# Performance work log

Hardware: AMD Instinct MI355X
Metric: run time of the kernel (lower is better)

## Reference

```python
import jax, jax.numpy as jnp
import numpy as np

MAX_LENGTH = 25
SOS_TOKEN = 0


def setup_inputs() -> dict:
    key = jax.random.key(0)
    B, S, H, V = 32, 50, 256, 50257
    ks = jax.random.split(key, 16)
    u = lambda k, shape, fan: jax.random.uniform(k, shape, jnp.float32, -1.0, 1.0) / np.sqrt(fan)
    return {
        "encoder_hidden": jax.random.normal(ks[0], (1, B, H), jnp.float32),
        "encoder_outputs": jax.random.normal(ks[1], (B, S, H), jnp.float32),
        "target_tensor": jax.random.randint(ks[2], (B, MAX_LENGTH), 0, V),
        "embedding": jax.random.normal(ks[3], (V, H), jnp.float32) * 0.02,
        "Wa_w": u(ks[4], (H, H), H), "Wa_b": u(ks[5], (H,), H),
        "Ua_w": u(ks[6], (H, H), H), "Ua_b": u(ks[7], (H,), H),
        "Va_w": u(ks[8], (1, H), H), "Va_b": u(ks[9], (1,), H),
        "gru_w_ih": u(ks[10], (3 * H, 2 * H), H), "gru_b_ih": u(ks[11], (3 * H,), H),
        "gru_w_hh": u(ks[12], (3 * H, H), H), "gru_b_hh": u(ks[13], (3 * H,), H),
        "out_w": u(ks[14], (V, H), H), "out_b": u(ks[15], (V,), H),
    }


def reference(encoder_hidden, encoder_outputs, target_tensor, embedding,
              Wa_w, Wa_b, Ua_w, Ua_b, Va_w, Va_b,
              gru_w_ih, gru_b_ih, gru_w_hh, gru_b_hh, out_w, out_b):
    B, S, H = encoder_outputs.shape
    keys = encoder_outputs
    # Ua(keys) is step-invariant: precompute.  [B,S,H]
    ua_keys = jnp.einsum("bsh,gh->bsg", keys, Ua_w) + Ua_b
    # teacher-forced input tokens: [SOS, target[:, :-1]] -> [T,B]
    toks = jnp.concatenate(
        [jnp.full((B, 1), SOS_TOKEN, dtype=target_tensor.dtype),
         target_tensor[:, : MAX_LENGTH - 1]], axis=1).T

    def step(h, tok):
        # h: [B,H], tok: [B]
        emb = embedding[tok]                                   # [B,H]
        # Bahdanau attention (dropout is identity in eval mode)
        wa_q = h @ Wa_w.T + Wa_b                               # [B,H]
        e = jnp.tanh(wa_q[:, None, :] + ua_keys)               # [B,S,H]
        scores = jnp.einsum("bsh,h->bs", e, Va_w[0]) + Va_b[0]  # [B,S]
        w = jax.nn.softmax(scores, axis=-1)                    # [B,S]
        ctx = jnp.einsum("bs,bsh->bh", w, keys)                # [B,H]
        # GRU cell (PyTorch gate order: r, z, n)
        x = jnp.concatenate([emb, ctx], axis=-1)               # [B,2H]
        gi = x @ gru_w_ih.T + gru_b_ih                         # [B,3H]
        gh = h @ gru_w_hh.T + gru_b_hh                         # [B,3H]
        ir, iz, inn = jnp.split(gi, 3, axis=-1)
        hr, hz, hn = jnp.split(gh, 3, axis=-1)
        r = jax.nn.sigmoid(ir + hr)
        z = jax.nn.sigmoid(iz + hz)
        n = jnp.tanh(inn + r * hn)
        h2 = (1.0 - z) * n + z * h
        logits = h2 @ out_w.T + out_b                          # [B,V]
        return h2, (logits, w)

    h0 = encoder_hidden[0]                                     # [B,H]
    hT, (logits, attn) = jax.lax.scan(step, h0, toks)          # [T,B,V], [T,B,S]
    dec_out = jax.nn.log_softmax(logits.transpose(1, 0, 2), axis=-1)  # [B,T,V]
    attentions = attn.transpose(1, 0, 2)                       # [B,T,S]
    return dec_out, hT[None], attentions
```

## Files before the change

### kernel.cpp

```cpp
#include <hip/hip_runtime.h>
#include <math.h>

#define B_ 32
#define S_ 50
#define H_ 256
#define T_ 25
#define V_ 50257
#define VP 50260
#define NCH 786
#define NROW (B_ * T_)
#define NWROW 1024
#define VT_ 3144
#define MROW 54
#define SOS 0

typedef unsigned short ushort_t;
typedef __attribute__((ext_vector_type(8))) unsigned short ushort8;
typedef __attribute__((ext_vector_type(8))) short short8v;
typedef __attribute__((ext_vector_type(4))) float f32x4;

__device__ ushort_t g_ua[B_ * S_ * H_];
__device__ ushort_t g_hbf[NROW * H_];
__device__ float    g_gie[T_ * B_ * 3 * H_];
__device__ ushort_t g_wpk[(size_t)VT_ * 32 * 16 * 8];
__device__ ushort_t g_wcat[NWROW * H_];
__device__ ushort_t g_MT2[B_ * 768 * MROW];
__device__ ushort_t g_lgt[(size_t)NROW * VP];
__device__ float    g_pmax[NROW * NCH];
__device__ float    g_psum[NROW * NCH];

__device__ __forceinline__ float bf2f(ushort_t h) {
  union { unsigned int u; float f; } c; c.u = ((unsigned int)h) << 16; return c.f;
}
__device__ __forceinline__ ushort_t f2bf(float f) {
  union { float f; unsigned int u; } c; c.f = f;
  unsigned int u = c.u;
  return (ushort_t)((u + 0x7FFFu + ((u >> 16) & 1u)) >> 16);
}
__device__ __forceinline__ float tanh_fast(float x) {
  const float e = __expf(2.f * x);
  return 1.f - 2.f / (e + 1.f);
}

__global__ void k_pre(const float* __restrict__ keys, const float* __restrict__ Ua_w,
                      const float* __restrict__ Ua_b, const float* __restrict__ Wa_b,
                      const float* __restrict__ W_hh, const float* __restrict__ Wa_w,
                      const float* __restrict__ W_ih, const float* __restrict__ b_ih,
                      const int* __restrict__ tgt, const float* __restrict__ emb_tab) {
  __shared__ float sbuf[S_ * H_];
  const int bid = blockIdx.x, tid = threadIdx.x;

  if (bid < B_ * S_) {
    sbuf[tid] = keys[bid * H_ + tid];
    __syncthreads();
    float acc = Ua_b[tid] + Wa_b[tid];
    const float4* wrow = (const float4*)(Ua_w + (size_t)tid * H_);
    const float4* sk4 = (const float4*)sbuf;
    for (int k = 0; k < H_ / 4; ++k) {
      const float4 w = wrow[k], x = sk4[k];
      acc += w.x * x.x + w.y * x.y + w.z * x.z + w.w * x.w;
    }
    g_ua[(size_t)bid * H_ + tid] = f2bf(acc);
  } else if (bid < 1984) {
    const int cc = bid - 1600;
    const int c = cc % 12, b = cc / 12;
    {
      const float4* src = (const float4*)(keys + (size_t)b * S_ * H_);
      float4* dst = (float4*)sbuf;
      for (int i = tid; i < S_ * H_ / 4; i += 256) dst[i] = src[i];
    }
    __syncthreads();
    const int sub = tid & 15, grp = tid >> 4;
#pragma unroll 1
    for (int it = 0; it < 4; ++it) {
      const int j = c * 64 + it * 16 + grp;
      float w16[16];
#pragma unroll
      for (int kp = 0; kp < 16; ++kp)
        w16[kp] = W_ih[(size_t)j * (2 * H_) + H_ + sub + 16 * kp];
#pragma unroll 1
      for (int s = 0; s < S_; ++s) {
        float a = 0.f;
#pragma unroll
        for (int kp = 0; kp < 16; ++kp) a += w16[kp] * sbuf[s * H_ + sub + 16 * kp];
        a += __shfl_xor(a, 8); a += __shfl_xor(a, 4);
        a += __shfl_xor(a, 2); a += __shfl_xor(a, 1);
        if (sub == 0) g_MT2[(size_t)b * 768 * MROW + j * MROW + s] = f2bf(a);
      }
    }
  } else if (bid < 2284) {
    const int cc = bid - 1984;
    const int chunk = cc % 12, t = cc / 12;
    for (int i = tid; i < B_ * H_; i += 256) {
      const int b = i >> 8, g = i & 255;
      const int tok = (t == 0) ? SOS : tgt[b * T_ + (t - 1)];
      sbuf[i] = emb_tab[(size_t)tok * H_ + g];
    }
    __syncthreads();
    const int vl = tid & 63, wd = tid >> 6;
    const int j = chunk * 64 + vl;
    const float4* wrow = (const float4*)(W_ih + (size_t)j * (2 * H_));
    const float4* se4 = (const float4*)sbuf;
    float acc[8];
    const float base = b_ih[j];
#pragma unroll
    for (int bb = 0; bb < 8; ++bb) acc[bb] = base;
    for (int k4 = 0; k4 < 64; ++k4) {
      const float4 w = wrow[k4];
#pragma unroll
      for (int bb = 0; bb < 8; ++bb) {
        const float4 x = se4[(wd * 8 + bb) * 64 + k4];
        acc[bb] += w.x * x.x + w.y * x.y + w.z * x.z + w.w * x.w;
      }
    }
#pragma unroll
    for (int bb = 0; bb < 8; ++bb)
      g_gie[((size_t)t * B_ + (wd * 8 + bb)) * (3 * H_) + j] = acc[bb];
  } else {
    const size_t i0 = (size_t)(bid - 2284) * 256 + tid;
    for (size_t i = i0; i < (size_t)NWROW * H_; i += 256u * 256u) {
      const int r = (int)(i >> 8), k = (int)(i & 255);
      const float v = (r < 256) ? Wa_w[r * H_ + k] : W_hh[(r - 256) * H_ + k];
      g_wcat[i] = f2bf(v);
    }
  }
}

__global__ void __launch_bounds__(1024, 1)
k_recur(const float* __restrict__ enc_h, const float* __restrict__ Va_w,
        const float* __restrict__ Va_b, const float* __restrict__ b_hh,
        const float* __restrict__ out_w, float* __restrict__ out) {
  __shared__ ushort_t s_ua[S_ * H_];
  __shared__ ushort_t s_M[768 * MROW];
  __shared__ float s_res[NWROW];
  __shared__ float s_mw[768];
  __shared__ float s_h[H_];
  __shared__ float s_va[H_];
  __shared__ float s_score[64], s_w[64];
  const int bidx = blockIdx.x, tid = threadIdx.x;

  if (bidx >= 32) {
    const size_t total = (size_t)VT_ * 32 * 16;
    for (size_t p = (size_t)(bidx - 32) * 1024 + tid; p < total;
         p += (size_t)(gridDim.x - 32) * 1024) {
      const int c = (int)(p & 15);
      const int kg = (int)((p >> 4) & 31);
      const int vt = (int)(p >> 9);
      const int v = vt * 16 + c;
      short8v val = {0, 0, 0, 0, 0, 0, 0, 0};
      if (v < V_) {
        const float4* owr = (const float4*)(out_w + (size_t)v * H_ + kg * 8);
        const float4 f0 = owr[0], f1 = owr[1];
        val[0] = (short)f2bf(f0.x); val[1] = (short)f2bf(f0.y);
        val[2] = (short)f2bf(f0.z); val[3] = (short)f2bf(f0.w);
        val[4] = (short)f2bf(f1.x); val[5] = (short)f2bf(f1.y);
        val[6] = (short)f2bf(f1.z); val[7] = (short)f2bf(f1.w);
      }
      ((short8v*)g_wpk)[p] = val;
    }
    return;
  }

  const int b = bidx;
  const int lane = tid & 63, wid = tid >> 6;
  const int sub = lane & 15;
  const int grp = tid >> 4;

  {
    const uint4* src = (const uint4*)(g_ua + (size_t)b * S_ * H_);
    uint4* dst = (uint4*)s_ua;
    for (int i = tid; i < S_ * H_ / 8; i += 1024) dst[i] = src[i];
    const uint4* src2 = (const uint4*)(g_MT2 + (size_t)b * 768 * MROW);
    uint4* dst2 = (uint4*)s_M;
    for (int i = tid; i < 768 * MROW / 8; i += 1024) dst2[i] = src2[i];
  }
  float hreg = 0.f, bhh0 = 0.f, bhh1 = 0.f, bhh2 = 0.f;
  if (tid < H_) {
    hreg = enc_h[b * H_ + tid];
    s_h[tid] = hreg;
    s_va[tid] = Va_w[tid];
    bhh0 = b_hh[tid]; bhh1 = b_hh[H_ + tid]; bhh2 = b_hh[2 * H_ + tid];
  }
  if (tid >= 50 && tid < 64) s_w[tid] = 0.f;
  const float vab = Va_b[0];
  __syncthreads();

  for (int t = 0; t < T_; ++t) {
    float gie0 = 0.f, gie1 = 0.f, gie2 = 0.f;
    if (tid < H_) {
      const float* gp = g_gie + ((size_t)t * B_ + b) * (3 * H_);
      gie0 = gp[tid]; gie1 = gp[H_ + tid]; gie2 = gp[2 * H_ + tid];
    }

#pragma unroll 4
    for (int it = 0; it < 16; ++it) {
      const int row = it * 64 + grp;
      const ushort8* wr = (const ushort8*)(g_wcat + (size_t)row * H_);
      const ushort8 w0 = wr[sub], w1 = wr[16 + sub];
      const float* v0 = s_h + sub * 8;
      const float* v1 = s_h + 128 + sub * 8;
      float a0 = 0.f, a1 = 0.f;
#pragma unroll
      for (int j = 0; j < 8; ++j) { a0 += bf2f(w0[j]) * v0[j]; a1 += bf2f(w1[j]) * v1[j]; }
      float a = a0 + a1;
      a += __shfl_xor(a, 8); a += __shfl_xor(a, 4);
      a += __shfl_xor(a, 2); a += __shfl_xor(a, 1);
      if (sub == 0) s_res[row] = a;
    }
    __syncthreads();

    for (int s = wid; s < S_; s += 16) {
      const ushort_t* uarow = s_ua + s * H_;
      float acc = 0.f;
#pragma unroll
      for (int i = 0; i < 4; ++i) {
        const int gg = lane + i * 64;
        acc += tanh_fast(s_res[gg] + bf2f(uarow[gg])) * s_va[gg];
      }
      for (int off = 32; off > 0; off >>= 1) acc += __shfl_xor(acc, off);
      if (lane == 0) s_score[s] = acc + vab;
    }
    __syncthreads();

    if (tid < 64) {
      const float v = (tid < S_) ? s_score[tid] : -INFINITY;
      float m = v;
      for (int off = 32; off > 0; off >>= 1) m = fmaxf(m, __shfl_xor(m, off));
      const float e = (tid < S_) ? __expf(v - m) : 0.f;
      float ssum = e;
      for (int off = 32; off > 0; off >>= 1) ssum += __shfl_xor(ssum, off);
      const float w = e / ssum;
      if (tid < S_) {
        s_w[tid] = w;
        out[(size_t)B_ * T_ * V_ + (size_t)B_ * H_ + (size_t)(b * T_ + t) * S_ + tid] = w;
      }
    }
    __syncthreads();

    if (tid < 768) {
      const unsigned int* m32 = (const unsigned int*)s_M + tid * (MROW / 2);
      float acc = 0.f;
#pragma unroll
      for (int i = 0; i < 25; ++i) {
        const unsigned int mv = m32[i];
        acc += bf2f((ushort_t)(mv & 0xffffu)) * s_w[2 * i];
        acc += bf2f((ushort_t)(mv >> 16)) * s_w[2 * i + 1];
      }
      s_mw[tid] = acc;
    }
    __syncthreads();

    if (tid < H_) {
      const float gi0 = gie0 + s_mw[tid];
      const float gi1 = gie1 + s_mw[H_ + tid];
      const float gi2 = gie2 + s_mw[2 * H_ + tid];
      const float gh0 = s_res[256 + tid] + bhh0;
      const float gh1 = s_res[512 + tid] + bhh1;
      const float gh2 = s_res[768 + tid] + bhh2;
      const float r = 1.f / (1.f + __expf(-(gi0 + gh0)));
      const float z = 1.f / (1.f + __expf(-(gi1 + gh1)));
      const float n = tanh_fast(gi2 + r * gh2);
      const float h2 = (1.f - z) * n + z * hreg;
      hreg = h2;
      s_h[tid] = h2;
      g_hbf[((size_t)b * T_ + t) * H_ + tid] = f2bf(h2);
      if (t == T_ - 1) out[(size_t)B_ * T_ * V_ + b * H_ + tid] = h2;
    }
    __syncthreads();
  }
}

__global__ void __launch_bounds__(256, 2)
k_logits(const float* __restrict__ out_b) {
  __shared__ ushort_t sA[128 * 256];
  const int tid = threadIdx.x;
  const int n0 = blockIdx.x * 128, m0 = blockIdx.y * 128;
  const int lane = tid & 63, wv = tid >> 6;
  const int wm = wv >> 1, wn = wv & 1;
  const int l16 = lane & 15, l4 = lane >> 4;

  for (int i = tid; i < 128 * 32; i += 256) {
    const int row = i >> 5, ks = i & 31;
    const int m = m0 + row;
    ushort8 val;
    if (m < NROW) val = ((const ushort8*)(g_hbf + (size_t)m * H_))[ks];
    else { ushort8 z = {0, 0, 0, 0, 0, 0, 0, 0}; val = z; }
    *(ushort8*)((char*)sA + row * 512 + ((ks ^ (row & 7)) << 4)) = val;
  }
  __syncthreads();

  f32x4 acc[4][4];
#pragma unroll
  for (int mi = 0; mi < 4; ++mi)
#pragma unroll
    for (int ni = 0; ni < 4; ++ni) acc[mi][ni] = (f32x4){0.f, 0.f, 0.f, 0.f};

  const int vt0 = (blockIdx.x << 3) + (wn << 2);
#pragma unroll 1
  for (int kk = 0; kk < 8; ++kk) {
    short8v a[4], bfr[4];
#pragma unroll
    for (int mi = 0; mi < 4; ++mi) {
      const int row = wm * 64 + mi * 16 + l16;
      const int ks = kk * 4 + l4;
      a[mi] = *(const short8v*)((const char*)sA + row * 512 + ((ks ^ (row & 7)) << 4));
    }
#pragma unroll
    for (int ni = 0; ni < 4; ++ni) {
      bfr[ni] = ((const short8v*)g_wpk)[(((size_t)(vt0 + ni) * 32) + kk * 4 + l4) * 16 + l16];
    }
#pragma unroll
    for (int mi = 0; mi < 4; ++mi)
#pragma unroll
      for (int ni = 0; ni < 4; ++ni)
        acc[mi][ni] = __builtin_amdgcn_mfma_f32_16x16x32_bf16(a[mi], bfr[ni], acc[mi][ni], 0, 0, 0);
  }

  int vcol[4]; float bias[4]; bool valid[4];
#pragma unroll
  for (int ni = 0; ni < 4; ++ni) {
    vcol[ni] = n0 + wn * 64 + ni * 16 + l16;
    valid[ni] = (vcol[ni] < V_);
    bias[ni] = valid[ni] ? out_b[vcol[ni]] : 0.f;
  }
  const int chunk = blockIdx.x * 2 + wn;
#pragma unroll
  for (int mi = 0; mi < 4; ++mi) {
#pragma unroll
    for (int j = 0; j < 4; ++j) {
      const int m = m0 + wm * 64 + mi * 16 + l4 * 4 + j;
      float vv[4];
      float mx = -INFINITY;
#pragma unroll
      for (int ni = 0; ni < 4; ++ni) {
        vv[ni] = acc[mi][ni][j] + bias[ni];
        if (valid[ni]) mx = fmaxf(mx, vv[ni]);
      }
      mx = fmaxf(mx, __shfl_xor(mx, 1)); mx = fmaxf(mx, __shfl_xor(mx, 2));
      mx = fmaxf(mx, __shfl_xor(mx, 4)); mx = fmaxf(mx, __shfl_xor(mx, 8));
      float es = 0.f;
#pragma unroll
      for (int ni = 0; ni < 4; ++ni) if (valid[ni]) es += __expf(vv[ni] - mx);
      es += __shfl_xor(es, 1); es += __shfl_xor(es, 2);
      es += __shfl_xor(es, 4); es += __shfl_xor(es, 8);
      if (m < NROW) {
#pragma unroll
        for (int ni = 0; ni < 4; ++ni)
          if (valid[ni]) g_lgt[(size_t)m * VP + vcol[ni]] = f2bf(vv[ni]);
        if (l16 == 0) {
          g_pmax[(size_t)m * NCH + chunk] = mx;
          g_psum[(size_t)m * NCH + chunk] = es;
        }
      }
    }
  }
}

__global__ void k_wlse(float* __restrict__ out) {
  __shared__ float red[4];
  const int r = blockIdx.x;
  const int tid = threadIdx.x;
  float m = -INFINITY;
  for (int i = tid; i < NCH; i += 256) m = fmaxf(m, g_pmax[(size_t)r * NCH + i]);
  for (int off = 32; off > 0; off >>= 1) m = fmaxf(m, __shfl_xor(m, off));
  if ((tid & 63) == 0) red[tid >> 6] = m;
  __syncthreads();
  m = fmaxf(fmaxf(red[0], red[1]), fmaxf(red[2], red[3]));
  __syncthreads();
  float s = 0.f;
  for (int i = tid; i < NCH; i += 256)
    s += g_psum[(size_t)r * NCH + i] * __expf(g_pmax[(size_t)r * NCH + i] - m);
  for (int off = 32; off > 0; off >>= 1) s += __shfl_xor(s, off);
  if ((tid & 63) == 0) red[tid >> 6] = s;
  __syncthreads();
  s = red[0] + red[1] + red[2] + red[3];
  float lse = m + logf(s);
  if (!isfinite(lse)) lse = 0.f;
  const size_t obase = (size_t)r * V_;
  const unsigned int* row32 = (const unsigned int*)(g_lgt + (size_t)r * VP);
#pragma unroll 1
  for (int i = tid; i < V_ / 2; i += 256) {
    const unsigned int u = row32[i];
    out[obase + 2 * i]     = bf2f((ushort_t)(u & 0xffffu)) - lse;
    out[obase + 2 * i + 1] = bf2f((ushort_t)(u >> 16)) - lse;
  }
  if (tid == 0)
    out[obase + V_ - 1] = bf2f(g_lgt[(size_t)r * VP + V_ - 1]) - lse;
}

extern "C" void kernel_launch(void* const* d_in, const int* in_sizes, int n_in,
                              void* d_out, int out_size, void* d_ws, size_t ws_size,
                              hipStream_t stream) {
  const float* enc_h  = (const float*)d_in[0];
  const float* keys   = (const float*)d_in[1];
  const int*   tgt    = (const int*)d_in[2];
  const float* emb    = (const float*)d_in[3];
  const float* Wa_w   = (const float*)d_in[4];
  const float* Wa_b   = (const float*)d_in[5];
  const float* Ua_w   = (const float*)d_in[6];
  const float* Ua_b   = (const float*)d_in[7];
  const float* Va_w   = (const float*)d_in[8];
  const float* Va_b   = (const float*)d_in[9];
  const float* W_ih   = (const float*)d_in[10];
  const float* b_ih   = (const float*)d_in[11];
  const float* W_hh   = (const float*)d_in[12];
  const float* b_hh   = (const float*)d_in[13];
  const float* out_w  = (const float*)d_in[14];
  const float* out_b  = (const float*)d_in[15];
  float* out = (float*)d_out;
  (void)d_ws; (void)ws_size;

  hipLaunchKernelGGL(k_pre, dim3(2540), dim3(256), 0, stream,
                     keys, Ua_w, Ua_b, Wa_b, W_hh, Wa_w, W_ih, b_ih, tgt, emb);
  hipLaunchKernelGGL(k_recur, dim3(32 + 1792), dim3(1024), 0, stream,
                     enc_h, Va_w, Va_b, b_hh, out_w, out);
  hipLaunchKernelGGL(k_logits, dim3(393, 7), dim3(256), 0, stream, out_b);
  hipLaunchKernelGGL(k_wlse, dim3(NROW), dim3(256), 0, stream, out);
}
```

Before: 521.4 us.

## Keep output-weight tile in LDS and loop over row tiles in logits GEMM

The logits kernel now launches one 512-thread block per 128-column vocab tile. Each block stages that tile's packed bf16 weights into shared memory once and loops over all seven 128-row tiles of hidden states, so each weight tile is read from global memory once instead of seven times. The cost is one block per tile (393 blocks), 128 KB of LDS per block, and a serial loop over row tiles, which lowers occupancy and parallelism. Separately, the Ua precompute in k_pre now has 16-lane groups read coalesced weight rows and combine partial sums with shuffles, instead of each thread reading a strided row on its own.

```diff
diff --git a/kernel.cpp b/kernel.cpp
--- a/kernel.cpp
+++ b/kernel.cpp
@@ -52,15 +52,24 @@
 
   if (bid < B_ * S_) {
     sbuf[tid] = keys[bid * H_ + tid];
-    __syncthreads();
-    float acc = Ua_b[tid] + Wa_b[tid];
-    const float4* wrow = (const float4*)(Ua_w + (size_t)tid * H_);
-    const float4* sk4 = (const float4*)sbuf;
-    for (int k = 0; k < H_ / 4; ++k) {
-      const float4 w = wrow[k], x = sk4[k];
-      acc += w.x * x.x + w.y * x.y + w.z * x.z + w.w * x.w;
-    }
-    g_ua[(size_t)bid * H_ + tid] = f2bf(acc);
+    sbuf[H_ + tid] = Ua_b[tid] + Wa_b[tid];
+    __syncthreads();
+    const int sub = tid & 15, grp = tid >> 4;
+#pragma unroll 4
+    for (int it = 0; it < 16; ++it) {
+      const int row = it * 16 + grp;
+      const float4* wr = (const float4*)(Ua_w + (size_t)row * H_);
+      float a = 0.f;
+#pragma unroll
+      for (int st = 0; st < 4; ++st) {
+        const float4 w = wr[st * 16 + sub];
+        const float4 x = *(const float4*)(sbuf + st * 64 + sub * 4);
+        a += w.x * x.x + w.y * x.y + w.z * x.z + w.w * x.w;
+      }
+      a += __shfl_xor(a, 8); a += __shfl_xor(a, 4);
+      a += __shfl_xor(a, 2); a += __shfl_xor(a, 1);
+      if (sub == 0) g_ua[(size_t)bid * H_ + row] = f2bf(a + sbuf[H_ + row]);
+    }
   } else if (bid < 1984) {
     const int cc = bid - 1600;
     const int c = cc % 12, b = cc / 12;
@@ -270,50 +279,20 @@
   }
 }
 
-__global__ void __launch_bounds__(256, 2)
+__global__ void __launch_bounds__(512, 1)
 k_logits(const float* __restrict__ out_b) {
   __shared__ ushort_t sA[128 * 256];
-  const int tid = threadIdx.x;
-  const int n0 = blockIdx.x * 128, m0 = blockIdx.y * 128;
+  __shared__ ushort_t sB[128 * 256];
+  const int tid = threadIdx.x, nb = blockIdx.x;
+  const int n0 = nb * 128;
   const int lane = tid & 63, wv = tid >> 6;
   const int wm = wv >> 1, wn = wv & 1;
   const int l16 = lane & 15, l4 = lane >> 4;
 
-  for (int i = tid; i < 128 * 32; i += 256) {
-    const int row = i >> 5, ks = i & 31;
-    const int m = m0 + row;
-    ushort8 val;
-    if (m < NROW) val = ((const ushort8*)(g_hbf + (size_t)m * H_))[ks];
-    else { ushort8 z = {0, 0, 0, 0, 0, 0, 0, 0}; val = z; }
-    *(ushort8*)((char*)sA + row * 512 + ((ks ^ (row & 7)) << 4)) = val;
-  }
-  __syncthreads();
-
-  f32x4 acc[4][4];
-#pragma unroll
-  for (int mi = 0; mi < 4; ++mi)
-#pragma unroll
-    for (int ni = 0; ni < 4; ++ni) acc[mi][ni] = (f32x4){0.f, 0.f, 0.f, 0.f};
-
-  const int vt0 = (blockIdx.x << 3) + (wn << 2);
-#pragma unroll 1
-  for (int kk = 0; kk < 8; ++kk) {
-    short8v a[4], bfr[4];
-#pragma unroll
-    for (int mi = 0; mi < 4; ++mi) {
-      const int row = wm * 64 + mi * 16 + l16;
-      const int ks = kk * 4 + l4;
-      a[mi] = *(const short8v*)((const char*)sA + row * 512 + ((ks ^ (row & 7)) << 4));
-    }
-#pragma unroll
-    for (int ni = 0; ni < 4; ++ni) {
-      bfr[ni] = ((const short8v*)g_wpk)[(((size_t)(vt0 + ni) * 32) + kk * 4 + l4) * 16 + l16];
-    }
-#pragma unroll
-    for (int mi = 0; mi < 4; ++mi)
-#pragma unroll
-      for (int ni = 0; ni < 4; ++ni)
-        acc[mi][ni] = __builtin_amdgcn_mfma_f32_16x16x32_bf16(a[mi], bfr[ni], acc[mi][ni], 0, 0, 0);
+  {
+    const short8v* src = (const short8v*)g_wpk + (size_t)nb * 4096;
+    short8v* dst = (short8v*)sB;
+    for (int i = tid; i < 4096; i += 512) dst[i] = src[i];
   }
 
   int vcol[4]; float bias[4]; bool valid[4];
@@ -323,33 +302,74 @@
     valid[ni] = (vcol[ni] < V_);
     bias[ni] = valid[ni] ? out_b[vcol[ni]] : 0.f;
   }
-  const int chunk = blockIdx.x * 2 + wn;
-#pragma unroll
-  for (int mi = 0; mi < 4; ++mi) {
-#pragma unroll
-    for (int j = 0; j < 4; ++j) {
-      const int m = m0 + wm * 64 + mi * 16 + l4 * 4 + j;
-      float vv[4];
-      float mx = -INFINITY;
-#pragma unroll
-      for (int ni = 0; ni < 4; ++ni) {
-        vv[ni] = acc[mi][ni][j] + bias[ni];
-        if (valid[ni]) mx = fmaxf(mx, vv[ni]);
-      }
-      mx = fmaxf(mx, __shfl_xor(mx, 1)); mx = fmaxf(mx, __shfl_xor(mx, 2));
-      mx = fmaxf(mx, __shfl_xor(mx, 4)); mx = fmaxf(mx, __shfl_xor(mx, 8));
-      float es = 0.f;
-#pragma unroll
-      for (int ni = 0; ni < 4; ++ni) if (valid[ni]) es += __expf(vv[ni] - mx);
-      es += __shfl_xor(es, 1); es += __shfl_xor(es, 2);
-      es += __shfl_xor(es, 4); es += __shfl_xor(es, 8);
-      if (m < NROW) {
+  const int chunk = nb * 2 + wn;
+
+#pragma unroll 1
+  for (int mt = 0; mt < 7; ++mt) {
+    const int m0 = mt * 128;
+    __syncthreads();
+    for (int i = tid; i < 128 * 32; i += 512) {
+      const int row = i >> 5, ks = i & 31;
+      const int m = m0 + row;
+      ushort8 val;
+      if (m < NROW) val = ((const ushort8*)(g_hbf + (size_t)m * H_))[ks];
+      else { ushort8 z = {0, 0, 0, 0, 0, 0, 0, 0}; val = z; }
+      *(ushort8*)((char*)sA + row * 512 + ((ks ^ (row & 7)) << 4)) = val;
+    }
+    __syncthreads();
+
+    f32x4 acc[2][4];
+#pragma unroll
+    for (int mi = 0; mi < 2; ++mi)
+#pragma unroll
+      for (int ni = 0; ni < 4; ++ni) acc[mi][ni] = (f32x4){0.f, 0.f, 0.f, 0.f};
+
+#pragma unroll 1
+    for (int kk = 0; kk < 8; ++kk) {
+      short8v a[2], bfr[4];
+#pragma unroll
+      for (int mi = 0; mi < 2; ++mi) {
+        const int row = wm * 32 + mi * 16 + l16;
+        const int ks = kk * 4 + l4;
+        a[mi] = *(const short8v*)((const char*)sA + row * 512 + ((ks ^ (row & 7)) << 4));
+      }
+#pragma unroll
+      for (int ni = 0; ni < 4; ++ni)
+        bfr[ni] = ((const short8v*)sB)[(((wn * 4 + ni) * 32) + kk * 4 + l4) * 16 + l16];
+#pragma unroll
+      for (int mi = 0; mi < 2; ++mi)
 #pragma unroll
         for (int ni = 0; ni < 4; ++ni)
-          if (valid[ni]) g_lgt[(size_t)m * VP + vcol[ni]] = f2bf(vv[ni]);
-        if (l16 == 0) {
-          g_pmax[(size_t)m * NCH + chunk] = mx;
-          g_psum[(size_t)m * NCH + chunk] = es;
+          acc[mi][ni] = __builtin_amdgcn_mfma_f32_16x16x32_bf16(a[mi], bfr[ni], acc[mi][ni], 0, 0, 0);
+    }
+
+#pragma unroll
+    for (int mi = 0; mi < 2; ++mi) {
+#pragma unroll
+      for (int j = 0; j < 4; ++j) {
+        const int m = m0 + wm * 32 + mi * 16 + l4 * 4 + j;
+        float vv[4];
+        float mx = -INFINITY;
+#pragma unroll
+        for (int ni = 0; ni < 4; ++ni) {
+          vv[ni] = acc[mi][ni][j] + bias[ni];
+          if (valid[ni]) mx = fmaxf(mx, vv[ni]);
+        }
+        mx = fmaxf(mx, __shfl_xor(mx, 1)); mx = fmaxf(mx, __shfl_xor(mx, 2));
+        mx = fmaxf(mx, __shfl_xor(mx, 4)); mx = fmaxf(mx, __shfl_xor(mx, 8));
+        float es = 0.f;
+#pragma unroll
+        for (int ni = 0; ni < 4; ++ni) if (valid[ni]) es += __expf(vv[ni] - mx);
+        es += __shfl_xor(es, 1); es += __shfl_xor(es, 2);
+        es += __shfl_xor(es, 4); es += __shfl_xor(es, 8);
+        if (m < NROW) {
+#pragma unroll
+          for (int ni = 0; ni < 4; ++ni)
+            if (valid[ni]) g_lgt[(size_t)m * VP + vcol[ni]] = f2bf(vv[ni]);
+          if (l16 == 0) {
+            g_pmax[(size_t)m * NCH + chunk] = mx;
+            g_psum[(size_t)m * NCH + chunk] = es;
+          }
         }
       }
     }
@@ -414,6 +434,6 @@
                      keys, Ua_w, Ua_b, Wa_b, W_hh, Wa_w, W_ih, b_ih, tgt, emb);
   hipLaunchKernelGGL(k_recur, dim3(32 + 1792), dim3(1024), 0, stream,
                      enc_h, Va_w, Va_b, b_hh, out_w, out);
-  hipLaunchKernelGGL(k_logits, dim3(393, 7), dim3(256), 0, stream, out_b);
+  hipLaunchKernelGGL(k_logits, dim3(393), dim3(512), 0, stream, out_b);
   hipLaunchKernelGGL(k_wlse, dim3(NROW), dim3(256), 0, stream, out);
 }
```

Measured after the change: 493.7 us. 1.06x faster.
